# Kernel tuning notes

Hardware: AMD Instinct MI355X
Metric: run time of the kernel (lower is better)

The kernel has to match this reference:

```python
import jax, jax.numpy as jnp
import numpy as np

GAMMA = 0.999      # EMA momentum
M_PROTO = 10       # prototypes per class
K_CLS = 201        # 200 classes + background
EPS_SK = 0.05      # sinkhorn temperature
SK_ITERS = 3       # sinkhorn iterations
THR = 0.5          # pseudo-gt threshold
D_BB = 768         # backbone dim
D = 512            # projected dim


def _ln(x, g, b, eps=1e-5):
    mu = x.mean(-1, keepdims=True)
    var = ((x - mu) ** 2).mean(-1, keepdims=True)
    return (x - mu) / jnp.sqrt(var + eps) * g + b


def _l2n(x, eps=1e-12):
    n = jnp.linalg.norm(x, axis=-1, keepdims=True)
    return x / jnp.maximum(n, eps)


def _pca_dir(A, niter=10):
    # rank-1 PCA direction (deterministic power iteration; mirrors torch.pca_lowrank(q=1, center=True))
    Ac = A - A.mean(0, keepdims=True)
    v = jnp.ones((A.shape[1],), A.dtype) / jnp.sqrt(jnp.asarray(A.shape[1], A.dtype))
    for _ in range(niter):
        v = Ac.T @ (Ac @ v)
        v = v / jnp.linalg.norm(v)
    u = Ac @ v
    return u / jnp.linalg.norm(u)


def setup_inputs() -> dict:
    key = jax.random.key(0)
    ks = jax.random.split(key, 6)
    B, HW = 16, 1024
    return dict(
        patch_tokens=jax.random.normal(ks[0], (B, HW, D_BB), jnp.float32),
        gt=jax.random.randint(ks[1], (B,), 0, K_CLS - 1),
        proj_w=jax.random.normal(ks[2], (D, D_BB), jnp.float32) * 0.02,
        proj_b=jnp.zeros((D,), jnp.float32),
        feat_g=jnp.ones((D,), jnp.float32),
        feat_b=jnp.zeros((D,), jnp.float32),
        mask_g=jnp.ones((K_CLS,), jnp.float32),
        mask_b=jnp.zeros((K_CLS,), jnp.float32),
        prototypes=jax.random.normal(ks[3], (K_CLS, M_PROTO, D), jnp.float32) * 0.02,
    )


def reference(patch_tokens, gt, proj_w, proj_b, feat_g, feat_b, mask_g, mask_b, prototypes):
    B, HW, _ = patch_tokens.shape
    H = W = int(np.sqrt(HW))
    N = B * HW

    # ----- ged_pseudo_gt (on detached tokens) -----
    U = _pca_dir(patch_tokens.reshape(-1, D_BB))            # [N]
    Us = (U - U.min()) / (U.max() - U.min())
    Us = Us.reshape(B, H, W)
    pseudo_gt = jnp.where(Us < THR, gt[:, None, None], K_CLS - 1)  # [B,H,W]

    # ----- projection + normalization -----
    f = patch_tokens @ proj_w.T + proj_b                    # [B,HW,D]
    _c = _l2n(_ln(f.reshape(N, D), feat_g, feat_b))         # [N,D]
    protos = _l2n(prototypes)                               # buffer is l2-normalized in-place
    masks = jnp.einsum('nd,kmd->nmk', _c, protos)           # [N,M,K] cosine sims
    out_flat = _ln(masks.max(axis=1), mask_g, mask_b)       # [N,K]
    out_seg = out_flat.reshape(B, H, W, K_CLS).transpose(0, 3, 1, 2)  # [B,K,H,W]

    # ----- prototype_learning (vectorized 201-class loop) -----
    gt_seg = pseudo_gt.reshape(-1)                          # [N] int
    pred = jnp.argmax(out_flat, axis=-1)
    correct = (gt_seg == pred).astype(_c.dtype)             # [N]
    proto_logits = _c @ protos.reshape(-1, D).T             # [N, K*M]

    sel = jax.nn.one_hot(gt_seg, K_CLS, dtype=_c.dtype)     # [N,K] class membership
    Bk = sel.sum(0)                                         # pixels per class
    Bk_safe = jnp.where(Bk > 0, Bk, 1.0)

    # masked per-class sinkhorn (all classes in parallel)
    Q = jnp.exp(masks / EPS_SK) * sel[:, None, :]           # [N,M,K]
    sQ = Q.sum((0, 1))                                      # [K]
    Q = Q / jnp.where(sQ > 0, sQ, 1.0)
    for _ in range(SK_ITERS):
        row = Q.sum(0, keepdims=True)                       # [1,M,K] sum over pixels
        Q = Q / jnp.where(row > 0, row, 1.0) / M_PROTO
        col = Q.sum(1, keepdims=True)                       # [N,1,K] sum over prototypes
        Q = Q / jnp.where(col > 0, col, 1.0) / Bk_safe
    Q = Q * Bk                                              # [N,M,K]

    Qn = jnp.take_along_axis(Q, gt_seg[:, None, None], axis=2)[:, :, 0]  # [N,M]
    idx = jnp.argmax(Qn, axis=1)                            # hard assignment per pixel
    proto_target = (idx + M_PROTO * gt_seg).astype(jnp.float32)

    # EMA update: q masked by prediction correctness (m_k applies to both m_q and c_q; m_k^2 = m_k)
    q = jax.nn.one_hot(idx, M_PROTO, dtype=_c.dtype) * correct[:, None]  # [N,M]
    fproto = jnp.einsum('nk,nm,nd->kmd', sel, q, _c)        # per-(class,proto) feature sums
    ncnt = jnp.einsum('nk,nm->km', sel, q)                  # assignment counts
    fnorm = _l2n(fproto)
    upd = (ncnt != 0)[:, :, None]
    new_protos = _l2n(jnp.where(upd, GAMMA * protos + (1.0 - GAMMA) * fnorm, protos))

    return out_seg, proto_logits, proto_target, pseudo_gt, new_protos
```

## Files before the change

### kernel.cpp

```cpp
#include <hip/hip_runtime.h>
#include <cstdint>
#include <cstddef>

typedef _Float16 half8  __attribute__((ext_vector_type(8)));
typedef _Float16 half4v __attribute__((ext_vector_type(4)));
typedef float    f32x4  __attribute__((ext_vector_type(4)));

static constexpr int HWPX = 1024;
static constexpr int NPX  = 16384;
static constexpr int DBB  = 768;
static constexpr int DD   = 512;
static constexpr int KC   = 201;
static constexpr int KM   = 2010;
static constexpr int KMP  = 2048;

static constexpr size_t OFF_MEANP  = 0;
static constexpr size_t OFF_XCH    = 49152;
static constexpr size_t OFF_ROW16  = 540672;
static constexpr size_t OFF_ROW3   = 669696;
static constexpr size_t OFF_ROW5   = 677760;
static constexpr size_t OFF_BK     = 685824;
static constexpr size_t OFF_NCNT   = 686848;
static constexpr size_t OFF_MM     = 694912;
static constexpr size_t OFF_FPROTO = 695296;
static constexpr size_t ZTOTAL     = 4811776;
static constexpr size_t OFF_GTSEG  = 4849664;
static constexpr size_t OFF_CORR   = 4915200;
static constexpr size_t OFF_U      = 4980736;
static constexpr size_t OFF_PN     = 5111808;
static constexpr size_t OFF_P16    = 9228288;
static constexpr size_t OFF_C16    = 11325440;
static constexpr size_t OFF_QD     = 28102656;
static constexpr size_t OFF_W16    = 28758016;
static constexpr size_t OFF_A16    = 29544448;

static constexpr size_t OUT_SEG = 0;
static constexpr size_t OUT_PL  = 3293184;
static constexpr size_t OUT_PT  = 36225024;
static constexpr size_t OUT_PG  = 36241408;
static constexpr size_t OUT_NP  = 36257792;

#define GLDS16(gp, lp) __builtin_amdgcn_global_load_lds( \
    (__attribute__((address_space(1))) const void*)(gp), \
    (__attribute__((address_space(3))) void*)(lp), 16, 0, 0)

static __device__ __forceinline__ float  wredf(float x){
  #pragma unroll
  for (int o=32;o;o>>=1) x += __shfl_down(x,o);
  return x;
}
static __device__ __forceinline__ double wredd(double x){
  #pragma unroll
  for (int o=32;o;o>>=1) x += __shfl_down(x,o);
  return x;
}

__global__ __launch_bounds__(256) void kP0(const float* __restrict__ A, double* __restrict__ meanp){
  __shared__ double red[4][12][64];
  int lane = threadIdx.x & 63, w = threadIdx.x >> 6;
  int rbase = blockIdx.x*16 + w*4;
  double acc[12];
  #pragma unroll
  for (int j=0;j<12;j++) acc[j]=0.0;
  for (int i=0;i<4;i++){
    const float* Ar = A + (size_t)(rbase+i)*DBB;
    #pragma unroll
    for (int j=0;j<12;j++) acc[j] += (double)Ar[j*64+lane];
  }
  #pragma unroll
  for (int j=0;j<12;j++) red[w][j][lane] = acc[j];
  __syncthreads();
  double* dst = meanp + (size_t)(blockIdx.x&7)*768;
  for (int cc=threadIdx.x; cc<768; cc+=256){
    int j = cc>>6, l = cc&63;
    double s = red[0][j][l]+red[1][j][l]+red[2][j][l]+red[3][j][l];
    atomicAdd(&dst[cc], s);
  }
}

__global__ __launch_bounds__(256) void kPIter(const float* __restrict__ A, const double* __restrict__ meanp,
                                              const double* __restrict__ xp, double* __restrict__ y){
  __shared__ double vs[768], ms[768];
  __shared__ double red[4][12][64];
  for (int cc=threadIdx.x; cc<768; cc+=256){
    double sm=0.0;
    #pragma unroll
    for (int p=0;p<8;p++) sm += meanp[p*768+cc];
    ms[cc] = sm * (1.0/16384.0);
    if (xp){
      double sv=0.0;
      #pragma unroll
      for (int p=0;p<8;p++) sv += xp[p*768+cc];
      vs[cc] = sv;
    } else {
      vs[cc] = 1.0/sqrt(768.0);
    }
  }
  __syncthreads();
  int lane = threadIdx.x & 63, w = threadIdx.x >> 6;
  int rbase = blockIdx.x*16 + w*4;
  double acc[12];
  #pragma unroll
  for (int j=0;j<12;j++) acc[j]=0.0;
  for (int i=0;i<4;i++){
    const float* Ar = A + (size_t)(rbase+i)*DBB;
    double ad[12]; double wp = 0.0;
    #pragma unroll
    for (int j=0;j<12;j++){ int c=j*64+lane; ad[j] = (double)Ar[c]-ms[c]; wp += ad[j]*vs[c]; }
    wp = wredd(wp); wp = __shfl(wp, 0);
    #pragma unroll
    for (int j=0;j<12;j++) acc[j] += wp*ad[j];
  }
  #pragma unroll
  for (int j=0;j<12;j++) red[w][j][lane] = acc[j];
  __syncthreads();
  double* dst = y + (size_t)(blockIdx.x&7)*768;
  for (int cc=threadIdx.x; cc<768; cc+=256){
    int j = cc>>6, l = cc&63;
    double s = red[0][j][l]+red[1][j][l]+red[2][j][l]+red[3][j][l];
    atomicAdd(&dst[cc], s);
  }
}

__global__ __launch_bounds__(256) void kPU(const float* __restrict__ A, const double* __restrict__ meanp,
                                           const double* __restrict__ vp, double* __restrict__ u){
  __shared__ double vs[768], ms[768];
  for (int cc=threadIdx.x; cc<768; cc+=256){
    double sm=0.0, sv=0.0;
    #pragma unroll
    for (int p=0;p<8;p++){ sm += meanp[p*768+cc]; sv += vp[p*768+cc]; }
    ms[cc] = sm * (1.0/16384.0);
    vs[cc] = sv;
  }
  __syncthreads();
  int lane=threadIdx.x&63, w=threadIdx.x>>6;
  int rbase = blockIdx.x*16 + w*4;
  for (int i=0;i<4;i++){
    const float* Ar = A + (size_t)(rbase+i)*DBB;
    double wp=0.0;
    #pragma unroll
    for (int j=0;j<12;j++){ int c=j*64+lane; wp += ((double)Ar[c]-ms[c])*vs[c]; }
    wp = wredd(wp);
    if (lane==0) u[rbase+i] = wp;
  }
}

__global__ __launch_bounds__(1024) void kMinMax(const double* __restrict__ u, double* __restrict__ mm){
  __shared__ double smn[16], smx[16];
  int t = threadIdx.x;
  double mn = 1e300, mx = -1e300;
  for (int i=t;i<NPX;i+=1024){ double x=u[i]; mn = fmin(mn,x); mx = fmax(mx,x); }
  #pragma unroll
  for (int o=32;o;o>>=1){ mn = fmin(mn, __shfl_down(mn,o)); mx = fmax(mx, __shfl_down(mx,o)); }
  if ((t&63)==0){ smn[t>>6]=mn; smx[t>>6]=mx; }
  __syncthreads();
  if (t==0){
    for (int i=1;i<16;i++){ mn=fmin(mn,smn[i]); mx=fmax(mx,smx[i]); }
    mm[0]=mn; mm[1]=mx;
  }
}

__global__ __launch_bounds__(256) void kPseudo(const double* __restrict__ u, const double* __restrict__ mm,
      const int* __restrict__ gt, float* __restrict__ outPG, int* __restrict__ gtseg, int* __restrict__ Bk){
  int n = blockIdx.x*256 + threadIdx.x;
  int b = n >> 10;
  double us = (u[n]-mm[0])/(mm[1]-mm[0]);
  int c0 = gt[b];
  int g = (us < 0.5) ? c0 : 200;
  outPG[n] = (float)g;
  gtseg[n] = g;
  unsigned long long b0 = __ballot(g==c0);
  unsigned long long b1 = __ballot(g==200);
  if ((threadIdx.x&63)==0){
    atomicAdd(&Bk[c0], (int)__popcll(b0));
    atomicAdd(&Bk[200], (int)__popcll(b1));
  }
}

__global__ __launch_bounds__(256) void kConv(const float* __restrict__ src, _Float16* __restrict__ dst, int n4){
  int stride = gridDim.x*256;
  for (int i = blockIdx.x*256+threadIdx.x; i<n4; i+=stride){
    float4 vv = ((const float4*)src)[i];
    half4v h; h[0]=(_Float16)vv.x; h[1]=(_Float16)vv.y; h[2]=(_Float16)vv.z; h[3]=(_Float16)vv.w;
    ((half4v*)dst)[i] = h;
  }
}

__global__ __launch_bounds__(256) void kProtoNorm(const float* __restrict__ PR, float* __restrict__ Pn,
                                                  _Float16* __restrict__ P16){
  int w=threadIdx.x>>6, lane=threadIdx.x&63;
  int km = blockIdx.x*4 + w;
  if (km >= KMP) return;
  if (km >= KM){
    half8 z;
    #pragma unroll
    for (int i=0;i<8;i++) z[i]=(_Float16)0.0f;
    *(half8*)(P16 + (size_t)km*DD + lane*8) = z;
    return;
  }
  const float* r = PR + (size_t)km*DD + lane*8;
  float4 a = *(const float4*)r, b2 = *(const float4*)(r+4);
  float x[8] = {a.x,a.y,a.z,a.w,b2.x,b2.y,b2.z,b2.w};
  float ss=0;
  #pragma unroll
  for (int i=0;i<8;i++) ss += x[i]*x[i];
  ss = __shfl(wredf(ss),0);
  float nrm = fmaxf(sqrtf(ss), 1e-12f);
  float* pw = Pn + (size_t)km*DD + lane*8;
  half8 h;
  #pragma unroll
  for (int i=0;i<8;i++){ float vv = x[i]/nrm; pw[i]=vv; h[i]=(_Float16)vv; }
  *(half8*)(P16 + (size_t)km*DD + lane*8) = h;
}

template<bool HALF_OUT>
__global__ __launch_bounds__(256) void gemm_f16(
    const _Float16* __restrict__ Am, const _Float16* __restrict__ Bm,
    float* __restrict__ Cf, _Float16* __restrict__ Ch,
    int Kd, int ldc, int ncols, const float* __restrict__ bias)
{
  __shared__ __align__(16) char As[128*128];
  __shared__ __align__(16) char Bs[128*128];
  const int tid = threadIdx.x;
  const int lane = tid & 63, w = tid >> 6;
  const int wr = w >> 1, wc = w & 1;
  const int lrow = lane & 15, kg = lane >> 4;
  const int m0 = blockIdx.x * 128, n0 = blockIdx.y * 128;

  f32x4 acc[4][4];
  #pragma unroll
  for (int i=0;i<4;i++)
    #pragma unroll
    for (int j=0;j<4;j++){ f32x4 z = {0.f,0.f,0.f,0.f}; acc[i][j]=z; }

  for (int k0 = 0; k0 < Kd; k0 += 64){
    #pragma unroll
    for (int i=0;i<4;i++){
      int slot = (i*4 + w)*64 + lane;
      int r = slot >> 3;
      int c = slot & 7;
      int cs = c ^ (r & 7);
      GLDS16(Am + (size_t)(m0+r)*Kd + k0 + cs*8, As + (i*4+w)*1024);
      GLDS16(Bm + (size_t)(n0+r)*Kd + k0 + cs*8, Bs + (i*4+w)*1024);
    }
    __syncthreads();
    #pragma unroll
    for (int h=0; h<2; h++){
      half8 af[4], bf[4];
      #pragma unroll
      for (int mi=0;mi<4;mi++){
        int ar = wr*64 + mi*16 + lrow;
        af[mi] = *(const half8*)(As + ar*128 + (((h*4+kg) ^ (ar&7))<<4));
      }
      #pragma unroll
      for (int nj=0;nj<4;nj++){
        int br = wc*64 + nj*16 + lrow;
        bf[nj] = *(const half8*)(Bs + br*128 + (((h*4+kg) ^ (br&7))<<4));
      }
      #pragma unroll
      for (int mi=0;mi<4;mi++)
        #pragma unroll
        for (int nj=0;nj<4;nj++)
          acc[mi][nj] = __builtin_amdgcn_mfma_f32_16x16x32_f16(af[mi], bf[nj], acc[mi][nj], 0,0,0);
    }
    __syncthreads();
  }
  #pragma unroll
  for (int mi=0;mi<4;mi++){
    int gr = m0 + wr*64 + mi*16 + kg*4;
    #pragma unroll
    for (int nj=0;nj<4;nj++){
      int gc = n0 + wc*64 + nj*16 + lrow;
      if (gc < ncols){
        float bv = bias ? bias[gc] : 0.0f;
        #pragma unroll
        for (int r2=0;r2<4;r2++){
          float vv = acc[mi][nj][r2] + bv;
          if (HALF_OUT) Ch[(size_t)(gr+r2)*ldc + gc] = (_Float16)vv;
          else          Cf[(size_t)(gr+r2)*ldc + gc] = vv;
        }
      }
    }
  }
}

__global__ __launch_bounds__(256) void kLNl2n(_Float16* __restrict__ C16,
      const float* __restrict__ fg, const float* __restrict__ fb){
  int w=threadIdx.x>>6, lane=threadIdx.x&63;
  int n = blockIdx.x*4 + w;
  _Float16* row = C16 + (size_t)n*DD + lane*8;
  half8 h = *(const half8*)row;
  float x[8];
  #pragma unroll
  for (int i=0;i<8;i++) x[i] = (float)h[i];
  float s=0;
  #pragma unroll
  for (int i=0;i<8;i++) s += x[i];
  float mu = __shfl(wredf(s),0)/512.f;
  float q=0;
  #pragma unroll
  for (int i=0;i<8;i++){ float d=x[i]-mu; q+=d*d; }
  float var = __shfl(wredf(q),0)/512.f;
  float inv = 1.f/sqrtf(var+1e-5f);
  float4 g0 = *(const float4*)(fg+lane*8), g1 = *(const float4*)(fg+lane*8+4);
  float4 b0 = *(const float4*)(fb+lane*8), b1 = *(const float4*)(fb+lane*8+4);
  float gg[8] = {g0.x,g0.y,g0.z,g0.w,g1.x,g1.y,g1.z,g1.w};
  float bb[8] = {b0.x,b0.y,b0.z,b0.w,b1.x,b1.y,b1.z,b1.w};
  float y[8]; float ss=0;
  #pragma unroll
  for (int i=0;i<8;i++){ y[i] = (x[i]-mu)*inv*gg[i]+bb[i]; ss += y[i]*y[i]; }
  float nrm = fmaxf(sqrtf(__shfl(wredf(ss),0)), 1e-12f);
  half8 o;
  #pragma unroll
  for (int i=0;i<8;i++) o[i] = (_Float16)(y[i]/nrm);
  *(half8*)row = o;
}

__global__ __launch_bounds__(256) void kMaxLNT(const float* __restrict__ PL, const float* __restrict__ mg,
    const float* __restrict__ mb, const int* __restrict__ gtseg,
    float* __restrict__ outseg, int* __restrict__ corr){
  __shared__ float rowb[4][2016];
  __shared__ float tile[32][205];
  int w=threadIdx.x>>6, lane=threadIdx.x&63;
  int n0 = blockIdx.x*32;
  int b = n0>>10, hw0 = n0&1023;
  for (int g8=0; g8<8; ++g8){
    int n = n0 + g8*4 + w;
    const float* src = PL + (size_t)n*KM;
    for (int j=lane;j<KM;j+=64) rowb[w][j] = src[j];
    float xv[4]; int ncl=0;
    for (int c=lane;c<KC;c+=64){
      float mx = rowb[w][c*10];
      #pragma unroll
      for (int m=1;m<10;m++) mx = fmaxf(mx, rowb[w][c*10+m]);
      xv[ncl++] = mx;
    }
    float ps=0;
    for (int i=0;i<ncl;i++) ps += xv[i];
    float mu = __shfl(wredf(ps),0)*(1.f/201.f);
    float pv=0;
    for (int i=0;i<ncl;i++){ float d=xv[i]-mu; pv+=d*d; }
    float var = __shfl(wredf(pv),0)*(1.f/201.f);
    float inv = 1.f/sqrtf(var+1e-5f);
    float bv = -3.0e38f; int bi = 1<<30;
    int lr = g8*4 + w;
    ncl = 0;
    for (int c=lane;c<KC;c+=64){
      float o = (xv[ncl]-mu)*inv*mg[c]+mb[c]; ncl++;
      tile[lr][c] = o;
      if (o > bv){ bv=o; bi=c; }
    }
    #pragma unroll
    for (int o2=32;o2;o2>>=1){
      float ov = __shfl_down(bv,o2); int oi = __shfl_down(bi,o2);
      if (ov>bv || (ov==bv && oi<bi)){ bv=ov; bi=oi; }
    }
    if (lane==0) corr[n] = (bi==gtseg[n]) ? 1 : 0;
  }
  __syncthreads();
  for (int idx=threadIdx.x; idx<KC*32; idx+=256){
    int c = idx>>5, j = idx&31;
    outseg[(((size_t)b*KC+c)<<10) + hw0 + j] = tile[j][c];
  }
}

__global__ __launch_bounds__(256) void kSKcosRow(const _Float16* __restrict__ C16, const _Float16* __restrict__ P16,
      const int* __restrict__ gtseg, const int* __restrict__ gt,
      float* __restrict__ Qd, float* __restrict__ row16){
  __shared__ double part[4][10][2];
  int w=threadIdx.x>>6, lane=threadIdx.x&63;
  int n = blockIdx.x*4+w;
  int g = gtseg[n];
  int c0 = gt[n>>10];
  half8 hc = *(const half8*)(C16 + (size_t)n*DD + lane*8);
  float c[8];
  #pragma unroll
  for (int i=0;i<8;i++) c[i]=(float)hc[i];
  const _Float16* Pb = P16 + (size_t)g*10*DD + lane*8;
  #pragma unroll
  for (int m=0;m<10;m++){
    half8 hp = *(const half8*)(Pb + m*DD);
    float d=0;
    #pragma unroll
    for (int i=0;i<8;i++) d += c[i]*(float)hp[i];
    float qv = wredf(d);
    if (lane==0){
      float e = expf(qv*20.f);
      Qd[(size_t)n*10+m] = e;
      part[w][m][0] = (g==c0)? (double)e : 0.0;
      part[w][m][1] = (g==200)? (double)e : 0.0;
    }
  }
  __syncthreads();
  if (threadIdx.x < 20){
    int m = threadIdx.x>>1, cl = threadIdx.x&1;
    double t = part[0][m][cl]+part[1][m][cl]+part[2][m][cl]+part[3][m][cl];
    atomicAdd(&row16[(size_t)(blockIdx.x&15)*2016 + m*KC + (cl?200:c0)], (float)t);
  }
}

__global__ __launch_bounds__(256) void kSKpass(float* __restrict__ Qd, const int* __restrict__ gtseg,
      const int* __restrict__ gt, const float* __restrict__ rin, int rin_parts,
      float* __restrict__ rout, const int* __restrict__ Bk){
  __shared__ float rin2[10][2];
  __shared__ double part[4][10][2];
  int n = blockIdx.x*256+threadIdx.x;
  int c0 = gt[blockIdx.x>>2];
  if (threadIdx.x < 20){
    int m = threadIdx.x>>1, cl = threadIdx.x&1;
    int cls = cl?200:c0;
    float s=0;
    for (int p=0;p<rin_parts;p++) s += rin[(size_t)p*2016 + m*KC + cls];
    rin2[m][cl]=s;
  }
  __syncthreads();
  int g = gtseg[n];
  int cl = (g==200)?1:0;
  double q[10]; double col=0.0;
  #pragma unroll
  for (int m=0;m<10;m++){
    double r = (double)rin2[m][cl];
    double t = (double)Qd[(size_t)n*10+m];
    if (r>0.0) t = t/r;
    t = t/10.0;
    q[m]=t; col+=t;
  }
  double cs = (col>0.0)? col : 1.0;
  int bk = Bk[g];
  double bs = (bk>0)? (double)bk : 1.0;
  double inv = 1.0/(cs*bs);
  int w=threadIdx.x>>6, lane=threadIdx.x&63;
  #pragma unroll
  for (int m=0;m<10;m++){
    double t = q[m]*inv;
    Qd[(size_t)n*10+m] = (float)t;
    double p0 = (g==c0)? t:0.0;
    double p1 = (g==200)? t:0.0;
    p0=wredd(p0); p1=wredd(p1);
    if (lane==0){ part[w][m][0]=p0; part[w][m][1]=p1; }
  }
  __syncthreads();
  if (threadIdx.x < 20){
    int m = threadIdx.x>>1, cl2 = threadIdx.x&1;
    double t = part[0][m][cl2]+part[1][m][cl2]+part[2][m][cl2]+part[3][m][cl2];
    atomicAdd(&rout[m*KC + (cl2?200:c0)], (float)t);
  }
}

__global__ __launch_bounds__(256) void kSKEMA(const float* __restrict__ Qd, const int* __restrict__ gtseg,
      const float* __restrict__ r5, const int* __restrict__ corr, const _Float16* __restrict__ C16,
      float* __restrict__ outPT, float* __restrict__ fproto, int* __restrict__ ncnt){
  int w=threadIdx.x>>6, lane=threadIdx.x&63;
  int n = blockIdx.x*4+w;
  int g = gtseg[n];
  float tv = -1.0f;
  if (lane<10){
    float r = r5[lane*KC+g];
    float t = Qd[(size_t)n*10+lane];
    if (r>0.f) t = t/r;
    tv = t*0.1f;
  }
  float bv = tv; int bi = lane;
  #pragma unroll
  for (int o=8;o;o>>=1){
    float ov = __shfl_down(bv,o); int oi = __shfl_down(bi,o);
    if (ov>bv || (ov==bv && oi<bi)){ bv=ov; bi=oi; }
  }
  bi = __shfl(bi, 0);
  if (lane==0) outPT[n] = (float)(bi + 10*g);
  if (corr[n]){
    half8 hc = *(const half8*)(C16 + (size_t)n*DD + lane*8);
    float* dst = fproto + ((size_t)g*10+bi)*DD + lane*8;
    #pragma unroll
    for (int i=0;i<8;i++) atomicAdd(dst+i, (float)hc[i]);
    if (lane==0) atomicAdd(&ncnt[g*10+bi], 1);
  }
}

__global__ __launch_bounds__(256) void kEMAfin(const float* __restrict__ fproto, const int* __restrict__ ncnt,
     const float* __restrict__ Pn, float* __restrict__ outNP){
  int w=threadIdx.x>>6, lane=threadIdx.x&63;
  int km = blockIdx.x*4+w;
  if (km>=KM) return;
  const float* fr = fproto + (size_t)km*DD + lane*8;
  float fp[8]; float ss=0;
  #pragma unroll
  for (int i=0;i<8;i++){ fp[i]=fr[i]; ss+=fp[i]*fp[i]; }
  float n1 = fmaxf(sqrtf(__shfl(wredf(ss),0)), 1e-12f);
  int cnt = ncnt[km];
  const float* pr = Pn + (size_t)km*DD + lane*8;
  float t[8]; float s2=0;
  #pragma unroll
  for (int i=0;i<8;i++){
    float pv = pr[i];
    float tv = cnt ? (0.999f*pv + 0.001f*(fp[i]/n1)) : pv;
    t[i]=tv; s2+=tv*tv;
  }
  float n2 = fmaxf(sqrtf(__shfl(wredf(s2),0)), 1e-12f);
  float* dst = outNP + (size_t)km*DD + lane*8;
  #pragma unroll
  for (int i=0;i<8;i++) dst[i] = t[i]/n2;
}

extern "C" void kernel_launch(void* const* d_in, const int* in_sizes, int n_in,
                              void* d_out, int out_size, void* d_ws, size_t ws_size,
                              hipStream_t stream) {
  const float* A   = (const float*)d_in[0];
  const int*   gt  = (const int*)d_in[1];
  const float* Wp  = (const float*)d_in[2];
  const float* pb  = (const float*)d_in[3];
  const float* fg  = (const float*)d_in[4];
  const float* fb  = (const float*)d_in[5];
  const float* mg  = (const float*)d_in[6];
  const float* mb  = (const float*)d_in[7];
  const float* PR  = (const float*)d_in[8];
  float* out = (float*)d_out;
  char* ws = (char*)d_ws;

  double* meanp  = (double*)(ws+OFF_MEANP);
  double* xch    = (double*)(ws+OFF_XCH);
  float*  row16  = (float*)(ws+OFF_ROW16);
  float*  row3   = (float*)(ws+OFF_ROW3);
  float*  row5   = (float*)(ws+OFF_ROW5);
  int*    Bk     = (int*)(ws+OFF_BK);
  int*    ncnt   = (int*)(ws+OFF_NCNT);
  double* mm     = (double*)(ws+OFF_MM);
  float*  fproto = (float*)(ws+OFF_FPROTO);
  int*    gtseg  = (int*)(ws+OFF_GTSEG);
  int*    corr   = (int*)(ws+OFF_CORR);
  double* u      = (double*)(ws+OFF_U);
  float*  Pn     = (float*)(ws+OFF_PN);
  _Float16* P16  = (_Float16*)(ws+OFF_P16);
  _Float16* C16  = (_Float16*)(ws+OFF_C16);
  float*  Qd     = (float*)(ws+OFF_QD);
  _Float16* W16  = (_Float16*)(ws+OFF_W16);
  _Float16* A16  = (_Float16*)(ws+OFF_A16);

  hipMemsetAsync(ws, 0, ZTOTAL, stream);

  kP0<<<1024,256,0,stream>>>(A, meanp);
  for (int t=0;t<10;t++){
    const double* xp = (t==0)? nullptr : (xch + (size_t)(t-1)*8*768);
    kPIter<<<1024,256,0,stream>>>(A, meanp, xp, xch + (size_t)t*8*768);
  }
  kPU<<<1024,256,0,stream>>>(A, meanp, xch + (size_t)9*8*768, u);
  kMinMax<<<1,1024,0,stream>>>(u, mm);
  kPseudo<<<64,256,0,stream>>>(u, mm, gt, out+OUT_PG, gtseg, Bk);

  kConv<<<2048,256,0,stream>>>(A, A16, NPX*DBB/4);
  kConv<<<384,256,0,stream>>>(Wp, W16, DD*DBB/4);
  kProtoNorm<<<512,256,0,stream>>>(PR, Pn, P16);

  gemm_f16<true><<<dim3(128,4),256,0,stream>>>(A16, W16, nullptr, C16, DBB, DD, DD, pb);
  kLNl2n<<<4096,256,0,stream>>>(C16, fg, fb);

  gemm_f16<false><<<dim3(128,16),256,0,stream>>>(C16, P16, out+OUT_PL, nullptr, DD, KM, KM, nullptr);

  kMaxLNT<<<512,256,0,stream>>>(out+OUT_PL, mg, mb, gtseg, out+OUT_SEG, corr);

  kSKcosRow<<<4096,256,0,stream>>>(C16, P16, gtseg, gt, Qd, row16);
  kSKpass<<<64,256,0,stream>>>(Qd, gtseg, gt, row16, 16, row3, Bk);
  kSKpass<<<64,256,0,stream>>>(Qd, gtseg, gt, row3, 1, row5, Bk);
  kSKEMA<<<4096,256,0,stream>>>(Qd, gtseg, row5, corr, C16, out+OUT_PT, fproto, ncnt);

  kEMAfin<<<503,256,0,stream>>>(fproto, ncnt, Pn, out+OUT_NP);
}
```

Baseline: 406.2 us.

## Fuse PCA chain into cooperative kernel, fold fp16 conversion into GEMM, reuse logits

Replaces the 14 separate PCA, min/max and pseudo-label launches with one cooperative-grid kernel that uses grid.sync between power-iteration steps. The fp32→fp16 conversion of the activations moves into the first GEMM's tile loader, which removes the standalone A16 pass. Weight conversion and prototype normalisation are merged into one launch, and both GEMMs get XCD-aware block swizzling. The Sinkhorn initialisation now reads the already-computed proto logits instead of recomputing dot products. The costs are grid-sync overhead, lower occupancy for the cooperative kernel, and conversion work inside the GEMM inner loop.

```diff
diff --git a/kernel.cpp b/kernel.cpp
--- a/kernel.cpp
+++ b/kernel.cpp
@@ -1,6 +1,9 @@
 #include <hip/hip_runtime.h>
+#include <hip/hip_cooperative_groups.h>
 #include <cstdint>
 #include <cstddef>
+
+namespace cg = cooperative_groups;
 
 typedef _Float16 half8  __attribute__((ext_vector_type(8)));
 typedef _Float16 half4v __attribute__((ext_vector_type(4)));
@@ -22,8 +25,9 @@
 static constexpr size_t OFF_BK     = 685824;
 static constexpr size_t OFF_NCNT   = 686848;
 static constexpr size_t OFF_MM     = 694912;
-static constexpr size_t OFF_FPROTO = 695296;
-static constexpr size_t ZTOTAL     = 4811776;
+static constexpr size_t OFF_PMM    = 694928;
+static constexpr size_t OFF_FPROTO = 703488;
+static constexpr size_t ZTOTAL     = 4819968;
 static constexpr size_t OFF_GTSEG  = 4849664;
 static constexpr size_t OFF_CORR   = 4915200;
 static constexpr size_t OFF_U      = 4980736;
@@ -32,7 +36,6 @@
 static constexpr size_t OFF_C16    = 11325440;
 static constexpr size_t OFF_QD     = 28102656;
 static constexpr size_t OFF_W16    = 28758016;
-static constexpr size_t OFF_A16    = 29544448;
 
 static constexpr size_t OUT_SEG = 0;
 static constexpr size_t OUT_PL  = 3293184;
@@ -55,147 +58,165 @@
   return x;
 }
 
-__global__ __launch_bounds__(256) void kP0(const float* __restrict__ A, double* __restrict__ meanp){
-  __shared__ double red[4][12][64];
-  int lane = threadIdx.x & 63, w = threadIdx.x >> 6;
-  int rbase = blockIdx.x*16 + w*4;
-  double acc[12];
-  #pragma unroll
-  for (int j=0;j<12;j++) acc[j]=0.0;
-  for (int i=0;i<4;i++){
-    const float* Ar = A + (size_t)(rbase+i)*DBB;
-    #pragma unroll
-    for (int j=0;j<12;j++) acc[j] += (double)Ar[j*64+lane];
-  }
-  #pragma unroll
-  for (int j=0;j<12;j++) red[w][j][lane] = acc[j];
-  __syncthreads();
-  double* dst = meanp + (size_t)(blockIdx.x&7)*768;
-  for (int cc=threadIdx.x; cc<768; cc+=256){
-    int j = cc>>6, l = cc&63;
-    double s = red[0][j][l]+red[1][j][l]+red[2][j][l]+red[3][j][l];
-    atomicAdd(&dst[cc], s);
-  }
-}
-
-__global__ __launch_bounds__(256) void kPIter(const float* __restrict__ A, const double* __restrict__ meanp,
-                                              const double* __restrict__ xp, double* __restrict__ y){
+__global__ __launch_bounds__(256, 2) void kPCAcoop(const float* __restrict__ A, const int* __restrict__ gt,
+    double* __restrict__ meanp, double* __restrict__ xch, double* __restrict__ u,
+    double* __restrict__ mm, double* __restrict__ pmm,
+    float* __restrict__ outPG, int* __restrict__ gtseg, int* __restrict__ Bk){
+  cg::grid_group grid = cg::this_grid();
   __shared__ double vs[768], ms[768];
   __shared__ double red[4][12][64];
-  for (int cc=threadIdx.x; cc<768; cc+=256){
-    double sm=0.0;
-    #pragma unroll
-    for (int p=0;p<8;p++) sm += meanp[p*768+cc];
-    ms[cc] = sm * (1.0/16384.0);
-    if (xp){
-      double sv=0.0;
-      #pragma unroll
-      for (int p=0;p<8;p++) sv += xp[p*768+cc];
+  __shared__ double sA[16];
+  const int tid = threadIdx.x;
+  const int lane = tid & 63, w = tid >> 6;
+  const int bid = blockIdx.x;
+  const int rbase = bid*32 + w*8;
+
+  {
+    double acc[12];
+    #pragma unroll
+    for (int j=0;j<12;j++) acc[j]=0.0;
+    for (int i=0;i<8;i++){
+      const float* Ar = A + (size_t)(rbase+i)*DBB;
+      #pragma unroll
+      for (int j=0;j<12;j++) acc[j] += (double)Ar[j*64+lane];
+    }
+    #pragma unroll
+    for (int j=0;j<12;j++) red[w][j][lane] = acc[j];
+    __syncthreads();
+    double* dst = meanp + (size_t)(bid&7)*768;
+    for (int cc=tid; cc<768; cc+=256){
+      int j = cc>>6, l = cc&63;
+      atomicAdd(&dst[cc], red[0][j][l]+red[1][j][l]+red[2][j][l]+red[3][j][l]);
+    }
+  }
+  grid.sync();
+
+  for (int t=0;t<10;t++){
+    const double* xp = (t==0)? nullptr : (xch + (size_t)(t-1)*8*768);
+    double* y = xch + (size_t)t*8*768;
+    for (int cc=tid; cc<768; cc+=256){
+      double sm=0.0;
+      #pragma unroll
+      for (int p=0;p<8;p++) sm += meanp[p*768+cc];
+      ms[cc] = sm * (1.0/16384.0);
+      if (xp){
+        double sv=0.0;
+        #pragma unroll
+        for (int p=0;p<8;p++) sv += xp[p*768+cc];
+        vs[cc] = sv;
+      } else {
+        vs[cc] = 1.0/sqrt(768.0);
+      }
+    }
+    __syncthreads();
+    double acc[12];
+    #pragma unroll
+    for (int j=0;j<12;j++) acc[j]=0.0;
+    for (int i=0;i<8;i++){
+      const float* Ar = A + (size_t)(rbase+i)*DBB;
+      double ad[12]; double wp = 0.0;
+      #pragma unroll
+      for (int j=0;j<12;j++){ int c=j*64+lane; ad[j] = (double)Ar[c]-ms[c]; wp += ad[j]*vs[c]; }
+      wp = wredd(wp); wp = __shfl(wp, 0);
+      #pragma unroll
+      for (int j=0;j<12;j++) acc[j] += wp*ad[j];
+    }
+    #pragma unroll
+    for (int j=0;j<12;j++) red[w][j][lane] = acc[j];
+    __syncthreads();
+    double* dst = y + (size_t)(bid&7)*768;
+    for (int cc=tid; cc<768; cc+=256){
+      int j = cc>>6, l = cc&63;
+      atomicAdd(&dst[cc], red[0][j][l]+red[1][j][l]+red[2][j][l]+red[3][j][l]);
+    }
+    grid.sync();
+  }
+
+  {
+    const double* vp = xch + (size_t)9*8*768;
+    for (int cc=tid; cc<768; cc+=256){
+      double sm=0.0, sv=0.0;
+      #pragma unroll
+      for (int p=0;p<8;p++){ sm += meanp[p*768+cc]; sv += vp[p*768+cc]; }
+      ms[cc] = sm * (1.0/16384.0);
       vs[cc] = sv;
-    } else {
-      vs[cc] = 1.0/sqrt(768.0);
-    }
-  }
-  __syncthreads();
-  int lane = threadIdx.x & 63, w = threadIdx.x >> 6;
-  int rbase = blockIdx.x*16 + w*4;
-  double acc[12];
-  #pragma unroll
-  for (int j=0;j<12;j++) acc[j]=0.0;
-  for (int i=0;i<4;i++){
-    const float* Ar = A + (size_t)(rbase+i)*DBB;
-    double ad[12]; double wp = 0.0;
-    #pragma unroll
-    for (int j=0;j<12;j++){ int c=j*64+lane; ad[j] = (double)Ar[c]-ms[c]; wp += ad[j]*vs[c]; }
-    wp = wredd(wp); wp = __shfl(wp, 0);
-    #pragma unroll
-    for (int j=0;j<12;j++) acc[j] += wp*ad[j];
-  }
-  #pragma unroll
-  for (int j=0;j<12;j++) red[w][j][lane] = acc[j];
-  __syncthreads();
-  double* dst = y + (size_t)(blockIdx.x&7)*768;
-  for (int cc=threadIdx.x; cc<768; cc+=256){
-    int j = cc>>6, l = cc&63;
-    double s = red[0][j][l]+red[1][j][l]+red[2][j][l]+red[3][j][l];
-    atomicAdd(&dst[cc], s);
-  }
-}
-
-__global__ __launch_bounds__(256) void kPU(const float* __restrict__ A, const double* __restrict__ meanp,
-                                           const double* __restrict__ vp, double* __restrict__ u){
-  __shared__ double vs[768], ms[768];
-  for (int cc=threadIdx.x; cc<768; cc+=256){
-    double sm=0.0, sv=0.0;
-    #pragma unroll
-    for (int p=0;p<8;p++){ sm += meanp[p*768+cc]; sv += vp[p*768+cc]; }
-    ms[cc] = sm * (1.0/16384.0);
-    vs[cc] = sv;
-  }
-  __syncthreads();
-  int lane=threadIdx.x&63, w=threadIdx.x>>6;
-  int rbase = blockIdx.x*16 + w*4;
-  for (int i=0;i<4;i++){
-    const float* Ar = A + (size_t)(rbase+i)*DBB;
-    double wp=0.0;
-    #pragma unroll
-    for (int j=0;j<12;j++){ int c=j*64+lane; wp += ((double)Ar[c]-ms[c])*vs[c]; }
-    wp = wredd(wp);
-    if (lane==0) u[rbase+i] = wp;
-  }
-}
-
-__global__ __launch_bounds__(1024) void kMinMax(const double* __restrict__ u, double* __restrict__ mm){
-  __shared__ double smn[16], smx[16];
-  int t = threadIdx.x;
-  double mn = 1e300, mx = -1e300;
-  for (int i=t;i<NPX;i+=1024){ double x=u[i]; mn = fmin(mn,x); mx = fmax(mx,x); }
-  #pragma unroll
-  for (int o=32;o;o>>=1){ mn = fmin(mn, __shfl_down(mn,o)); mx = fmax(mx, __shfl_down(mx,o)); }
-  if ((t&63)==0){ smn[t>>6]=mn; smx[t>>6]=mx; }
-  __syncthreads();
-  if (t==0){
-    for (int i=1;i<16;i++){ mn=fmin(mn,smn[i]); mx=fmax(mx,smx[i]); }
-    mm[0]=mn; mm[1]=mx;
-  }
-}
-
-__global__ __launch_bounds__(256) void kPseudo(const double* __restrict__ u, const double* __restrict__ mm,
-      const int* __restrict__ gt, float* __restrict__ outPG, int* __restrict__ gtseg, int* __restrict__ Bk){
-  int n = blockIdx.x*256 + threadIdx.x;
-  int b = n >> 10;
-  double us = (u[n]-mm[0])/(mm[1]-mm[0]);
-  int c0 = gt[b];
-  int g = (us < 0.5) ? c0 : 200;
-  outPG[n] = (float)g;
-  gtseg[n] = g;
-  unsigned long long b0 = __ballot(g==c0);
-  unsigned long long b1 = __ballot(g==200);
-  if ((threadIdx.x&63)==0){
-    atomicAdd(&Bk[c0], (int)__popcll(b0));
-    atomicAdd(&Bk[200], (int)__popcll(b1));
-  }
-}
-
-__global__ __launch_bounds__(256) void kConv(const float* __restrict__ src, _Float16* __restrict__ dst, int n4){
-  int stride = gridDim.x*256;
-  for (int i = blockIdx.x*256+threadIdx.x; i<n4; i+=stride){
-    float4 vv = ((const float4*)src)[i];
+    }
+    __syncthreads();
+    for (int i=0;i<8;i++){
+      const float* Ar = A + (size_t)(rbase+i)*DBB;
+      double wp=0.0;
+      #pragma unroll
+      for (int j=0;j<12;j++){ int c=j*64+lane; wp += ((double)Ar[c]-ms[c])*vs[c]; }
+      wp = wredd(wp);
+      if (lane==0) u[rbase+i] = wp;
+    }
+  }
+  grid.sync();
+
+  {
+    double x = (tid<32)? u[bid*32+tid] : u[bid*32];
+    double mn = x, mx = x;
+    #pragma unroll
+    for (int o=32;o;o>>=1){ mn=fmin(mn,__shfl_down(mn,o)); mx=fmax(mx,__shfl_down(mx,o)); }
+    if ((tid&63)==0){ sA[(tid>>6)*2]=mn; sA[(tid>>6)*2+1]=mx; }
+    __syncthreads();
+    if (tid==0){
+      for (int i2=1;i2<4;i2++){ mn=fmin(mn,sA[i2*2]); mx=fmax(mx,sA[i2*2+1]); }
+      pmm[bid*2]=mn; pmm[bid*2+1]=mx;
+    }
+  }
+  grid.sync();
+  if (bid==0){
+    double mn = fmin(pmm[tid*2],   pmm[(tid+256)*2]);
+    double mx = fmax(pmm[tid*2+1], pmm[(tid+256)*2+1]);
+    #pragma unroll
+    for (int o=32;o;o>>=1){ mn=fmin(mn,__shfl_down(mn,o)); mx=fmax(mx,__shfl_down(mx,o)); }
+    __syncthreads();
+    if ((tid&63)==0){ sA[(tid>>6)*2]=mn; sA[(tid>>6)*2+1]=mx; }
+    __syncthreads();
+    if (tid==0){
+      for (int i2=1;i2<4;i2++){ mn=fmin(mn,sA[i2*2]); mx=fmax(mx,sA[i2*2+1]); }
+      mm[0]=mn; mm[1]=mx;
+    }
+  }
+  grid.sync();
+
+  if (tid < 32){
+    int n = bid*32 + tid;
+    int b = n >> 10;
+    double us = (u[n]-mm[0])/(mm[1]-mm[0]);
+    int c0g = gt[b];
+    int g = (us < 0.5) ? c0g : 200;
+    outPG[n] = (float)g;
+    gtseg[n] = g;
+    unsigned long long b0 = __ballot(g==c0g);
+    unsigned long long b1 = __ballot(g==200);
+    if (tid==0){
+      atomicAdd(&Bk[c0g], (int)__popcll(b0));
+      atomicAdd(&Bk[200], (int)__popcll(b1));
+    }
+  }
+}
+
+__global__ __launch_bounds__(256) void kPrep(const float* __restrict__ Wp, _Float16* __restrict__ W16,
+    const float* __restrict__ PR, float* __restrict__ Pn, _Float16* __restrict__ P16){
+  int b = blockIdx.x;
+  if (b < 384){
+    int i = b*256 + threadIdx.x;
+    float4 vv = ((const float4*)Wp)[i];
     half4v h; h[0]=(_Float16)vv.x; h[1]=(_Float16)vv.y; h[2]=(_Float16)vv.z; h[3]=(_Float16)vv.w;
-    ((half4v*)dst)[i] = h;
-  }
-}
-
-__global__ __launch_bounds__(256) void kProtoNorm(const float* __restrict__ PR, float* __restrict__ Pn,
-                                                  _Float16* __restrict__ P16){
+    ((half4v*)W16)[i] = h;
+    return;
+  }
   int w=threadIdx.x>>6, lane=threadIdx.x&63;
-  int km = blockIdx.x*4 + w;
-  if (km >= KMP) return;
+  int km = (b-384)*4 + w;
   if (km >= KM){
-    half8 z;
-    #pragma unroll
-    for (int i=0;i<8;i++) z[i]=(_Float16)0.0f;
-    *(half8*)(P16 + (size_t)km*DD + lane*8) = z;
+    if (km < KMP){
+      half8 z;
+      #pragma unroll
+      for (int i=0;i<8;i++) z[i]=(_Float16)0.0f;
+      *(half8*)(P16 + (size_t)km*DD + lane*8) = z;
+    }
     return;
   }
   const float* r = PR + (size_t)km*DD + lane*8;
@@ -213,19 +234,18 @@
   *(half8*)(P16 + (size_t)km*DD + lane*8) = h;
 }
 
-template<bool HALF_OUT>
-__global__ __launch_bounds__(256) void gemm_f16(
-    const _Float16* __restrict__ Am, const _Float16* __restrict__ Bm,
-    float* __restrict__ Cf, _Float16* __restrict__ Ch,
-    int Kd, int ldc, int ncols, const float* __restrict__ bias)
-{
+__global__ __launch_bounds__(256) void gemm1(const float* __restrict__ Af, const _Float16* __restrict__ Bm,
+    _Float16* __restrict__ Ch, const float* __restrict__ bias){
   __shared__ __align__(16) char As[128*128];
   __shared__ __align__(16) char Bs[128*128];
   const int tid = threadIdx.x;
   const int lane = tid & 63, w = tid >> 6;
   const int wr = w >> 1, wc = w & 1;
   const int lrow = lane & 15, kg = lane >> 4;
-  const int m0 = blockIdx.x * 128, n0 = blockIdx.y * 128;
+  const int id = blockIdx.x;
+  const int xcd = id & 7, pos = id >> 3;
+  const int m0 = ((xcd<<4) | (pos>>2)) * 128;
+  const int n0 = (pos & 3) * 128;
 
   f32x4 acc[4][4];
   #pragma unroll
@@ -233,15 +253,21 @@
     #pragma unroll
     for (int j=0;j<4;j++){ f32x4 z = {0.f,0.f,0.f,0.f}; acc[i][j]=z; }
 
-  for (int k0 = 0; k0 < Kd; k0 += 64){
+  for (int k0 = 0; k0 < DBB; k0 += 64){
     #pragma unroll
     for (int i=0;i<4;i++){
       int slot = (i*4 + w)*64 + lane;
-      int r = slot >> 3;
-      int c = slot & 7;
+      int r = slot >> 3, c = slot & 7;
       int cs = c ^ (r & 7);
-      GLDS16(Am + (size_t)(m0+r)*Kd + k0 + cs*8, As + (i*4+w)*1024);
-      GLDS16(Bm + (size_t)(n0+r)*Kd + k0 + cs*8, Bs + (i*4+w)*1024);
+      GLDS16(Bm + (size_t)(n0+r)*DBB + k0 + cs*8, Bs + (i*4+w)*1024);
+    }
+    #pragma unroll
+    for (int i=0;i<8;i++){
+      int slot = i*256 + tid;
+      int r = slot >> 4, c4 = slot & 15;
+      float4 v = *(const float4*)(Af + (size_t)(m0+r)*DBB + k0 + c4*4);
+      half4v h; h[0]=(_Float16)v.x; h[1]=(_Float16)v.y; h[2]=(_Float16)v.z; h[3]=(_Float16)v.w;
+      *(half4v*)(As + r*128 + (((c4>>1)^(r&7))<<4) + (c4&1)*8) = h;
     }
     __syncthreads();
     #pragma unroll
@@ -271,14 +297,74 @@
     #pragma unroll
     for (int nj=0;nj<4;nj++){
       int gc = n0 + wc*64 + nj*16 + lrow;
-      if (gc < ncols){
-        float bv = bias ? bias[gc] : 0.0f;
+      float bv = bias[gc];
+      #pragma unroll
+      for (int r2=0;r2<4;r2++)
+        Ch[(size_t)(gr+r2)*DD + gc] = (_Float16)(acc[mi][nj][r2] + bv);
+    }
+  }
+}
+
+__global__ __launch_bounds__(256) void gemm2(const _Float16* __restrict__ Am, const _Float16* __restrict__ Bm,
+    float* __restrict__ Cf){
+  __shared__ __align__(16) char As[128*128];
+  __shared__ __align__(16) char Bs[128*128];
+  const int tid = threadIdx.x;
+  const int lane = tid & 63, w = tid >> 6;
+  const int wr = w >> 1, wc = w & 1;
+  const int lrow = lane & 15, kg = lane >> 4;
+  const int id = blockIdx.x;
+  const int xcd = id & 7, pos = id >> 3;
+  const int m0 = ((xcd<<4) | (pos>>4)) * 128;
+  const int n0 = (pos & 15) * 128;
+
+  f32x4 acc[4][4];
+  #pragma unroll
+  for (int i=0;i<4;i++)
+    #pragma unroll
+    for (int j=0;j<4;j++){ f32x4 z = {0.f,0.f,0.f,0.f}; acc[i][j]=z; }
+
+  for (int k0 = 0; k0 < DD; k0 += 64){
+    #pragma unroll
+    for (int i=0;i<4;i++){
+      int slot = (i*4 + w)*64 + lane;
+      int r = slot >> 3, c = slot & 7;
+      int cs = c ^ (r & 7);
+      GLDS16(Am + (size_t)(m0+r)*DD + k0 + cs*8, As + (i*4+w)*1024);
+      GLDS16(Bm + (size_t)(n0+r)*DD + k0 + cs*8, Bs + (i*4+w)*1024);
+    }
+    __syncthreads();
+    #pragma unroll
+    for (int h=0; h<2; h++){
+      half8 af[4], bf[4];
+      #pragma unroll
+      for (int mi=0;mi<4;mi++){
+        int ar = wr*64 + mi*16 + lrow;
+        af[mi] = *(const half8*)(As + ar*128 + (((h*4+kg) ^ (ar&7))<<4));
+      }
+      #pragma unroll
+      for (int nj=0;nj<4;nj++){
+        int br = wc*64 + nj*16 + lrow;
+        bf[nj] = *(const half8*)(Bs + br*128 + (((h*4+kg) ^ (br&7))<<4));
+      }
+      #pragma unroll
+      for (int mi=0;mi<4;mi++)
         #pragma unroll
-        for (int r2=0;r2<4;r2++){
-          float vv = acc[mi][nj][r2] + bv;
-          if (HALF_OUT) Ch[(size_t)(gr+r2)*ldc + gc] = (_Float16)vv;
-          else          Cf[(size_t)(gr+r2)*ldc + gc] = vv;
-        }
+        for (int nj=0;nj<4;nj++)
+          acc[mi][nj] = __builtin_amdgcn_mfma_f32_16x16x32_f16(af[mi], bf[nj], acc[mi][nj], 0,0,0);
+    }
+    __syncthreads();
+  }
+  #pragma unroll
+  for (int mi=0;mi<4;mi++){
+    int gr = m0 + wr*64 + mi*16 + kg*4;
+    #pragma unroll
+    for (int nj=0;nj<4;nj++){
+      int gc = n0 + wc*64 + nj*16 + lrow;
+      if (gc < KM){
+        #pragma unroll
+        for (int r2=0;r2<4;r2++)
+          Cf[(size_t)(gr+r2)*KM + gc] = acc[mi][nj][r2];
       }
     }
   }
@@ -327,7 +413,8 @@
   for (int g8=0; g8<8; ++g8){
     int n = n0 + g8*4 + w;
     const float* src = PL + (size_t)n*KM;
-    for (int j=lane;j<KM;j+=64) rowb[w][j] = src[j];
+    for (int j2=lane;j2<1005;j2+=64)
+      *(float2*)(&rowb[w][j2*2]) = *(const float2*)(src + j2*2);
     float xv[4]; int ncl=0;
     for (int c=lane;c<KC;c+=64){
       float mx = rowb[w][c*10];
@@ -364,32 +451,33 @@
   }
 }
 
-__global__ __launch_bounds__(256) void kSKcosRow(const _Float16* __restrict__ C16, const _Float16* __restrict__ P16,
-      const int* __restrict__ gtseg, const int* __restrict__ gt,
-      float* __restrict__ Qd, float* __restrict__ row16){
+__global__ __launch_bounds__(256) void kSKgRow(const float* __restrict__ PL, const int* __restrict__ gtseg,
+      const int* __restrict__ gt, float* __restrict__ Qd, float* __restrict__ row16){
   __shared__ double part[4][10][2];
+  int n = blockIdx.x*256+threadIdx.x;
+  int g = gtseg[n];
+  int c0 = gt[blockIdx.x>>2];
   int w=threadIdx.x>>6, lane=threadIdx.x&63;
-  int n = blockIdx.x*4+w;
-  int g = gtseg[n];
-  int c0 = gt[n>>10];
-  half8 hc = *(const half8*)(C16 + (size_t)n*DD + lane*8);
-  float c[8];
-  #pragma unroll
-  for (int i=0;i<8;i++) c[i]=(float)hc[i];
-  const _Float16* Pb = P16 + (size_t)g*10*DD + lane*8;
+  const float* src = PL + (size_t)n*KM + g*10;
+  float e[10];
+  #pragma unroll
+  for (int m2=0;m2<5;m2++){
+    float2 v = *(const float2*)(src + m2*2);
+    e[m2*2]   = expf(v.x*20.f);
+    e[m2*2+1] = expf(v.y*20.f);
+  }
+  float* qdst = Qd + (size_t)n*10;
+  #pragma unroll
+  for (int m2=0;m2<5;m2++){
+    float2 v; v.x=e[m2*2]; v.y=e[m2*2+1];
+    *(float2*)(qdst + m2*2) = v;
+  }
   #pragma unroll
   for (int m=0;m<10;m++){
-    half8 hp = *(const half8*)(Pb + m*DD);
-    float d=0;
-    #pragma unroll
-    for (int i=0;i<8;i++) d += c[i]*(float)hp[i];
-    float qv = wredf(d);
-    if (lane==0){
-      float e = expf(qv*20.f);
-      Qd[(size_t)n*10+m] = e;
-      part[w][m][0] = (g==c0)? (double)e : 0.0;
-      part[w][m][1] = (g==200)? (double)e : 0.0;
-    }
+    double p0 = (g==c0)? (double)e[m]:0.0;
+    double p1 = (g==200)? (double)e[m]:0.0;
+    p0=wredd(p0); p1=wredd(p1);
+    if (lane==0){ part[w][m][0]=p0; part[w][m][1]=p1; }
   }
   __syncthreads();
   if (threadIdx.x < 20){
@@ -525,6 +613,7 @@
   int*    Bk     = (int*)(ws+OFF_BK);
   int*    ncnt   = (int*)(ws+OFF_NCNT);
   double* mm     = (double*)(ws+OFF_MM);
+  double* pmm    = (double*)(ws+OFF_PMM);
   float*  fproto = (float*)(ws+OFF_FPROTO);
   int*    gtseg  = (int*)(ws+OFF_GTSEG);
   int*    corr   = (int*)(ws+OFF_CORR);
@@ -534,31 +623,24 @@
   _Float16* C16  = (_Float16*)(ws+OFF_C16);
   float*  Qd     = (float*)(ws+OFF_QD);
   _Float16* W16  = (_Float16*)(ws+OFF_W16);
-  _Float16* A16  = (_Float16*)(ws+OFF_A16);
 
   hipMemsetAsync(ws, 0, ZTOTAL, stream);
 
-  kP0<<<1024,256,0,stream>>>(A, meanp);
-  for (int t=0;t<10;t++){
-    const double* xp = (t==0)? nullptr : (xch + (size_t)(t-1)*8*768);
-    kPIter<<<1024,256,0,stream>>>(A, meanp, xp, xch + (size_t)t*8*768);
-  }
-  kPU<<<1024,256,0,stream>>>(A, meanp, xch + (size_t)9*8*768, u);
-  kMinMax<<<1,1024,0,stream>>>(u, mm);
-  kPseudo<<<64,256,0,stream>>>(u, mm, gt, out+OUT_PG, gtseg, Bk);
-
-  kConv<<<2048,256,0,stream>>>(A, A16, NPX*DBB/4);
-  kConv<<<384,256,0,stream>>>(Wp, W16, DD*DBB/4);
-  kProtoNorm<<<512,256,0,stream>>>(PR, Pn, P16);
-
-  gemm_f16<true><<<dim3(128,4),256,0,stream>>>(A16, W16, nullptr, C16, DBB, DD, DD, pb);
+  float* outPG = out + OUT_PG;
+  void* args[] = {(void*)&A, (void*)&gt, (void*)&meanp, (void*)&xch, (void*)&u,
+                  (void*)&mm, (void*)&pmm, (void*)&outPG, (void*)&gtseg, (void*)&Bk};
+  hipLaunchCooperativeKernel((void*)kPCAcoop, dim3(512), dim3(256), args, 0, stream);
+
+  kPrep<<<896,256,0,stream>>>(Wp, W16, PR, Pn, P16);
+
+  gemm1<<<512,256,0,stream>>>(A, W16, C16, pb);
   kLNl2n<<<4096,256,0,stream>>>(C16, fg, fb);
 
-  gemm_f16<false><<<dim3(128,16),256,0,stream>>>(C16, P16, out+OUT_PL, nullptr, DD, KM, KM, nullptr);
+  gemm2<<<2048,256,0,stream>>>(C16, P16, out+OUT_PL);
 
   kMaxLNT<<<512,256,0,stream>>>(out+OUT_PL, mg, mb, gtseg, out+OUT_SEG, corr);
 
-  kSKcosRow<<<4096,256,0,stream>>>(C16, P16, gtseg, gt, Qd, row16);
+  kSKgRow<<<64,256,0,stream>>>(out+OUT_PL, gtseg, gt, Qd, row16);
   kSKpass<<<64,256,0,stream>>>(Qd, gtseg, gt, row16, 16, row3, Bk);
   kSKpass<<<64,256,0,stream>>>(Qd, gtseg, gt, row3, 1, row5, Bk);
   kSKEMA<<<4096,256,0,stream>>>(Qd, gtseg, row5, corr, C16, out+OUT_PT, fproto, ncnt);
```

Result: slower. 1.081 ms (+166.3%).
